# Performance work log

Measured on AMD Instinct MI355X. Metric: run time of the kernel, lower is better.

Reference implementation:

```python
import jax, jax.numpy as jnp
import numpy as np

H = 4            # heads
C = 64           # per-head dim (= hidden, PyG TransformerConv semantics)
HD = 64          # hidden_dim
L = 2            # num_layers
NT = 2           # node types: 0=task, 1=machine
ET = ((0, 1), (1, 0))  # edge types: (src_nt, dst_nt)
N = 16384        # nodes per type (== max_nodes -> simple pos-enc slice)
E = 262144       # edges per edge type


def _ln(x, g, b):
    mu = x.mean(-1, keepdims=True)
    var = ((x - mu) ** 2).mean(-1, keepdims=True)
    return (x - mu) * jax.lax.rsqrt(var + 1e-5) * g + b


def _tconv(x_src, x_dst, ei, Wq, bq, Wk, bk, Wv, bv, Ws, bs, Wb):
    # PyG TransformerConv: heads=H, out_channels=C, concat=False, beta=True
    n_dst = x_dst.shape[0]
    src, dst = ei[0], ei[1]
    q = (x_dst @ Wq + bq).reshape(-1, H, C)
    k = (x_src @ Wk + bk).reshape(-1, H, C)
    v = (x_src @ Wv + bv).reshape(-1, H, C)
    logits = jnp.einsum('ehc,ehc->eh', q[dst], k[src]) * (1.0 / float(np.sqrt(C)))  # [E,H]
    m = jax.ops.segment_max(logits, dst, num_segments=n_dst)          # [N,H] segment softmax
    ex = jnp.exp(logits - m[dst])
    denom = jax.ops.segment_sum(ex, dst, num_segments=n_dst)
    alpha = ex / denom[dst]                                            # [E,H]
    msg = (alpha[:, :, None] * v[src]).reshape(-1, H * C)              # [E,H*C]
    out = jax.ops.segment_sum(msg, dst, num_segments=n_dst)
    out = out.reshape(n_dst, H, C).mean(axis=1)                        # concat=False -> head mean
    r = x_dst @ Ws + bs                                                # lin_skip
    beta = jax.nn.sigmoid(jnp.concatenate([out, r, out - r], -1) @ Wb) # lin_beta, [N,1]
    return beta * r + (1.0 - beta) * out


def _forward(edge_index, x, W_in, b_in, type_emb, pos, Wq, bq, Wk, bk, Wv, bv,
             Wskip, bskip, Wbeta, ln_g, ln_b, ff_W1, ff_b1, ff_W2, ff_b2, W_out, b_out):
    # input proj + type embedding + positional encoding (num_nodes == max_nodes -> slice)
    h = [x[t] @ W_in[t] + b_in[t] + type_emb[t] + pos[t] for t in range(NT)]
    for l in range(L):
        hn = [jnp.zeros_like(h[0]), jnp.zeros_like(h[1])]
        for e, (s, d) in enumerate(ET):  # HeteroConv, aggr='sum'
            hn[d] = hn[d] + _tconv(h[s], h[d], edge_index[e],
                                   Wq[l, e], bq[l, e], Wk[l, e], bk[l, e],
                                   Wv[l, e], bv[l, e], Wskip[l, e], bskip[l, e], Wbeta[l, e])
        for t in range(NT):
            hr = _ln(h[t] + hn[t], ln_g[l, t], ln_b[l, t])
            ff = jax.nn.gelu(hr @ ff_W1[l, t] + ff_b1[l, t], approximate=False) @ ff_W2[l, t] + ff_b2[l, t]
            h[t] = hr + ff
    return jnp.stack([h[t] @ W_out[t] + b_out[t] for t in range(NT)])  # [NT,N,HD]


def setup_inputs() -> dict:
    key = jax.random.key(0)
    ks = jax.random.split(key, 16)
    w = lambda k, s: 0.02 * jax.random.normal(k, s, jnp.float32)
    NE = len(ET)
    return {
        'x': jax.random.normal(ks[0], (NT, N, HD), jnp.float32),
        'edge_index': jax.random.randint(ks[1], (NE, 2, E), 0, N, jnp.int32),
        'W_in': w(ks[2], (NT, HD, HD)), 'b_in': jnp.zeros((NT, HD), jnp.float32),
        'type_emb': w(ks[3], (NT, HD)),
        'pos': w(ks[4], (NT, N, HD)),
        'Wq': w(ks[5], (L, NE, HD, H * C)), 'bq': jnp.zeros((L, NE, H * C), jnp.float32),
        'Wk': w(ks[6], (L, NE, HD, H * C)), 'bk': jnp.zeros((L, NE, H * C), jnp.float32),
        'Wv': w(ks[7], (L, NE, HD, H * C)), 'bv': jnp.zeros((L, NE, H * C), jnp.float32),
        'Wskip': w(ks[8], (L, NE, HD, HD)), 'bskip': jnp.zeros((L, NE, HD), jnp.float32),
        'Wbeta': w(ks[9], (L, NE, 3 * HD, 1)),
        'ln_g': jnp.ones((L, NT, HD), jnp.float32), 'ln_b': jnp.zeros((L, NT, HD), jnp.float32),
        'ff_W1': w(ks[10], (L, NT, HD, 4 * HD)), 'ff_b1': jnp.zeros((L, NT, 4 * HD), jnp.float32),
        'ff_W2': w(ks[11], (L, NT, 4 * HD, HD)), 'ff_b2': jnp.zeros((L, NT, HD), jnp.float32),
        'W_out': w(ks[12], (NT, HD, HD)), 'b_out': jnp.zeros((NT, HD), jnp.float32),
    }


def reference(x, edge_index, W_in, b_in, type_emb, pos, Wq, bq, Wk, bk, Wv, bv,
              Wskip, bskip, Wbeta, ln_g, ln_b, ff_W1, ff_b1, ff_W2, ff_b2, W_out, b_out):
    return _forward(edge_index, x, W_in, b_in, type_emb, pos, Wq, bq, Wk, bk, Wv, bv,
                    Wskip, bskip, Wbeta, ln_g, ln_b, ff_W1, ff_b1, ff_W2, ff_b2, W_out, b_out)
```

## Files before the change

### kernel.cpp

```cpp
#include <hip/hip_runtime.h>
#include <math.h>

#define NN 16384
#define EE 262144

typedef __bf16 v8bf __attribute__((ext_vector_type(8)));
typedef __bf16 v4bf __attribute__((ext_vector_type(4)));
typedef float  v4f  __attribute__((ext_vector_type(4)));
typedef float  v2f  __attribute__((ext_vector_type(2)));

#define OFF_CNT     0
#define OFF_FILL    (2*NN)
#define OFF_ROWPTR  (4*NN)
#define OFF_COLSRC  98816
#define OFF_H       623104
#define OFF_HN      (OFF_H  + 2*NN*64)
#define OFF_Q       (OFF_HN + 2*NN*64)
#define OFF_KV      (OFF_Q  + 2*NN*128)
#define OFF_R       (OFF_KV + 2*NN*128)
#define OFF_WT      (OFF_R  + 2*NN*64)
#define OFF_WBP     (OFF_WT + 180224)
#define OFF_LNG     (OFF_WBP + 768)
#define OFF_LNB     (OFF_LNG + 256)


#define WT_Q   0
#define WT_K   65536
#define WT_V   131072
#define WT_S   196608
#define WT_IN  212992
#define WT_W1  221184
#define WT_W2  286720
#define WT_WO  352256

__device__ __forceinline__ float blo(unsigned u) { return __uint_as_float(u << 16); }
__device__ __forceinline__ float bhi(unsigned u) { return __uint_as_float(u & 0xffff0000u); }
__device__ __forceinline__ unsigned short f2b(float f) {
  __bf16 h = (__bf16)f;
  return *(unsigned short*)&h;
}

struct PrepDesc { const float* src; unsigned short* dst; int ksh; int total; int kperm; };
struct PrepPack { PrepDesc d[28]; };

__global__ __launch_bounds__(256) void prep_kernel(PrepPack p) {
  PrepDesc g = p.d[blockIdx.y];
  int idx = blockIdx.x * 256 + threadIdx.x;
  if (idx >= g.total) return;
  int K = 1 << g.ksh;
  int n = idx >> g.ksh;
  int k = idx & (K - 1);
  int N = g.total >> g.ksh;
  int kk = g.kperm ? (16 * (k & 3) + (k >> 2)) : k;
  g.dst[idx] = f2b(g.src[(size_t)kk * N + n]);
}

struct PermDesc { const float* src; float* dst; int total; };
struct PermPack { PermDesc d[3]; };

__global__ __launch_bounds__(256) void perm_kernel(PermPack p) {
  PermDesc g = p.d[blockIdx.y];
  int idx = blockIdx.x * 256 + threadIdx.x;
  if (idx >= g.total) return;
  int c = idx & 63;
  g.dst[(idx & ~63) + ((c & 15) << 2) + (c >> 4)] = g.src[idx];
}

__global__ void count_kernel(const int* __restrict__ ei, int* __restrict__ cnt) {
  int idx = blockIdx.x * 256 + threadIdx.x;
  if (idx >= 2 * EE) return;
  int et = idx >> 18;
  int j  = idx & (EE - 1);
  int dst = ei[et * 2 * EE + EE + j];
  atomicAdd(&cnt[et * NN + dst], 1);
}

__global__ __launch_bounds__(1024) void scan_kernel(const int* __restrict__ cnt,
                                                    int* __restrict__ rowptr,
                                                    int* __restrict__ fill) {
  int et = blockIdx.x;
  const int* c = cnt + et * NN;
  __shared__ int sums[1024];
  int tid = threadIdx.x;
  int base = tid * 16;
  int loc[16];
  int s = 0;
#pragma unroll
  for (int i = 0; i < 16; ++i) { loc[i] = s; s += c[base + i]; }
  sums[tid] = s;
  __syncthreads();
  for (int off = 1; off < 1024; off <<= 1) {
    int v = 0;
    if (tid >= off) v = sums[tid - off];
    __syncthreads();
    if (tid >= off) sums[tid] += v;
    __syncthreads();
  }
  int ebase = (tid == 0) ? 0 : sums[tid - 1];
  int* rp = rowptr + et * (NN + 1);
  int* fl = fill + et * NN;
#pragma unroll
  for (int i = 0; i < 16; ++i) {
    rp[base + i] = ebase + loc[i];
    fl[base + i] = ebase + loc[i];
  }
  if (tid == 1023) rp[NN] = sums[1023];
}

__global__ void scatter_kernel(const int* __restrict__ ei, int* __restrict__ fill,
                               int* __restrict__ colsrc) {
  int idx = blockIdx.x * 256 + threadIdx.x;
  if (idx >= 2 * EE) return;
  int et = idx >> 18;
  int j  = idx & (EE - 1);
  int src = ei[et * 2 * EE + j];
  int dst = ei[et * 2 * EE + EE + j];
  int pos = atomicAdd(&fill[et * NN + dst], 1);
  colsrc[et * EE + pos] = (et * NN + src) << 9;
}

struct GemmDesc {
  const float *A, *bias, *bias2, *add;
  const unsigned short* Bt;
  char* C;
  int Ncols, Cld, ntiles, gelu, otype;
};
struct GemmPack { GemmDesc d[8]; int nd; };

#define LDA 72

__global__ __launch_bounds__(256) void gemm_mfma(GemmPack p) {
  GemmDesc g = p.d[blockIdx.y];
  const int row0 = blockIdx.x * 128;
  const int tid = threadIdx.x;
  const int w = tid >> 6, lane = tid & 63;
  const int l16 = lane & 15, quad = lane >> 4;

  __shared__ __bf16 As[128 * LDA];
  __shared__ __bf16 Bs[64 * LDA];

#pragma unroll
  for (int it = 0; it < 8; ++it) {
    int fi = it * 256 + tid;
    int grow = fi >> 4;
    int kq = (fi & 15) << 2;
    float4 a = *(const float4*)(g.A + (size_t)(row0 + grow) * 64 + kq);
    v4bf c = { (__bf16)a.x, (__bf16)a.y, (__bf16)a.z, (__bf16)a.w };
    *(v4bf*)&As[grow * LDA + kq] = c;
  }

  const int brow = tid >> 2;
  const int bko  = (tid & 3) << 4;

  for (int ct0 = 0; ct0 < g.ntiles; ++ct0) {
    const int col0 = ct0 * 64;
    __syncthreads();
    {
      const unsigned short* bp = g.Bt + (size_t)(col0 + brow) * 64 + bko;
      uint4 b0 = *(const uint4*)(bp);
      uint4 b1 = *(const uint4*)(bp + 8);
      *(uint4*)&Bs[brow * LDA + bko] = b0;
      *(uint4*)&Bs[brow * LDA + bko + 8] = b1;
    }
    __syncthreads();

    v4f acc[2][4];
#pragma unroll
    for (int rt = 0; rt < 2; ++rt)
#pragma unroll
      for (int ct = 0; ct < 4; ++ct)
#pragma unroll
        for (int r = 0; r < 4; ++r) acc[rt][ct][r] = 0.f;

#pragma unroll
    for (int ks = 0; ks < 2; ++ks) {
      v8bf a0 = *(v8bf*)&As[(w * 32 + l16) * LDA + ks * 32 + quad * 8];
      v8bf a1 = *(v8bf*)&As[(w * 32 + 16 + l16) * LDA + ks * 32 + quad * 8];
#pragma unroll
      for (int ct = 0; ct < 4; ++ct) {
        v8bf bb = *(v8bf*)&Bs[(ct * 16 + l16) * LDA + ks * 32 + quad * 8];
        acc[0][ct] = __builtin_amdgcn_mfma_f32_16x16x32_bf16(a0, bb, acc[0][ct], 0, 0, 0);
        acc[1][ct] = __builtin_amdgcn_mfma_f32_16x16x32_bf16(a1, bb, acc[1][ct], 0, 0, 0);
      }
    }

    float bias_c[4];
#pragma unroll
    for (int ct = 0; ct < 4; ++ct) {
      int col = col0 + ct * 16 + l16;
      float b = g.bias ? g.bias[col] : 0.f;
      if (g.bias2) b += g.bias2[col];
      bias_c[ct] = b;
    }
#pragma unroll
    for (int rt = 0; rt < 2; ++rt)
#pragma unroll
      for (int r = 0; r < 4; ++r) {
        size_t row = row0 + w * 32 + rt * 16 + quad * 4 + r;
        char* cp = g.C + row * (size_t)g.Cld;
        if (g.otype == 0) {
          float vv[4];
#pragma unroll
          for (int ct = 0; ct < 4; ++ct) {
            int col = col0 + ct * 16 + l16;
            float v = acc[rt][ct][r] + bias_c[ct];
            if (g.add) v += g.add[row * g.Ncols + col];
            if (g.gelu) v = 0.5f * v * (1.f + erff(v * 0.70710678118654752f));
            vv[ct] = v;
          }
          float4 w4 = { vv[0], vv[1], vv[2], vv[3] };
          *(float4*)(cp + col0 * 4 + l16 * 16) = w4;
        } else if (g.otype == 1) {
          ushort4 wq;
          wq.x = f2b(acc[rt][0][r] + bias_c[0]);
          wq.y = f2b(acc[rt][1][r] + bias_c[1]);
          wq.z = f2b(acc[rt][2][r] + bias_c[2]);
          wq.w = f2b(acc[rt][3][r] + bias_c[3]);
          *(ushort4*)(cp + col0 * 2 + l16 * 8) = wq;
        } else {
          unsigned wv = 0;
#pragma unroll
          for (int ct = 0; ct < 4; ++ct) {
            float v = acc[rt][ct][r] + bias_c[ct];
            unsigned pk = __builtin_amdgcn_cvt_pk_fp8_f32(v, v, 0, false);
            wv |= (pk & 0xffu) << (8 * ct);
          }
          *(unsigned*)(cp + col0 + l16 * 4) = wv;
        }
      }
  }
}

struct FFPack {
  const float *HN;
  const unsigned short *W1t, *W2t, *Wot;
  const float *b1, *b2, *bout;
  float* H;
  float* outbuf;
};

__global__ __launch_bounds__(256) void ff_fused(FFPack p) {
  const int t = blockIdx.y;
  const int row0 = blockIdx.x * 64;
  const int tid = threadIdx.x;
  const int w = tid >> 6, lane = tid & 63;
  const int l16 = lane & 15, quad = lane >> 4;

  const float* A  = p.HN + ((size_t)t * NN) * 64;
  const unsigned short* W1t = p.W1t + (size_t)t * 16384;
  const unsigned short* W2t = p.W2t + (size_t)t * 16384;
  const float* b1 = p.b1 + t * 256;
  const float* b2 = p.b2 + t * 64;

  __shared__ __bf16 As[64 * LDA];
  __shared__ __bf16 A2[64 * LDA];
  __shared__ __bf16 B1s[64 * LDA];
  __shared__ __bf16 B2s[64 * LDA];

#pragma unroll
  for (int it = 0; it < 4; ++it) {
    int fi = it * 256 + tid;
    int grow = fi >> 4;
    int kq = (fi & 15) << 2;
    float4 a = *(const float4*)(A + (size_t)(row0 + grow) * 64 + kq);
    v4bf c = { (__bf16)a.x, (__bf16)a.y, (__bf16)a.z, (__bf16)a.w };
    *(v4bf*)&As[grow * LDA + kq] = c;
  }

  const int brow = tid >> 2;
  const int bko  = (tid & 3) << 4;

  v4f acc2[4];
#pragma unroll
  for (int ct = 0; ct < 4; ++ct)
#pragma unroll
    for (int r = 0; r < 4; ++r) acc2[ct][r] = 0.f;

  for (int c1 = 0; c1 < 4; ++c1) {
    {
      const unsigned short* bp1 = W1t + (size_t)(c1 * 64 + brow) * 64 + bko;
      uint4 u0 = *(const uint4*)(bp1);
      uint4 u1 = *(const uint4*)(bp1 + 8);
      *(uint4*)&B1s[brow * LDA + bko] = u0;
      *(uint4*)&B1s[brow * LDA + bko + 8] = u1;
      const unsigned short* bp2 = W2t + (size_t)brow * 256 + c1 * 64 + bko;
      uint4 u2 = *(const uint4*)(bp2);
      uint4 u3 = *(const uint4*)(bp2 + 8);
      *(uint4*)&B2s[brow * LDA + bko] = u2;
      *(uint4*)&B2s[brow * LDA + bko + 8] = u3;
    }
    __syncthreads();

    v4f acc1[4];
#pragma unroll
    for (int ct = 0; ct < 4; ++ct)
#pragma unroll
      for (int r = 0; r < 4; ++r) acc1[ct][r] = 0.f;
#pragma unroll
    for (int ks = 0; ks < 2; ++ks) {
      v8bf a = *(v8bf*)&As[(w * 16 + l16) * LDA + ks * 32 + quad * 8];
#pragma unroll
      for (int ct = 0; ct < 4; ++ct) {
        v8bf bb = *(v8bf*)&B1s[(ct * 16 + l16) * LDA + ks * 32 + quad * 8];
        acc1[ct] = __builtin_amdgcn_mfma_f32_16x16x32_bf16(a, bb, acc1[ct], 0, 0, 0);
      }
    }
#pragma unroll
    for (int ct = 0; ct < 4; ++ct) {
      float bb = b1[c1 * 64 + ct * 16 + l16];
#pragma unroll
      for (int r = 0; r < 4; ++r) {
        float v = acc1[ct][r] + bb;
        v = 0.5f * v * (1.f + erff(v * 0.70710678118654752f));
        A2[(w * 16 + quad * 4 + r) * LDA + ct * 16 + l16] = (__bf16)v;
      }
    }
#pragma unroll
    for (int ks = 0; ks < 2; ++ks) {
      v8bf a = *(v8bf*)&A2[(w * 16 + l16) * LDA + ks * 32 + quad * 8];
#pragma unroll
      for (int ct = 0; ct < 4; ++ct) {
        v8bf bb = *(v8bf*)&B2s[(ct * 16 + l16) * LDA + ks * 32 + quad * 8];
        acc2[ct] = __builtin_amdgcn_mfma_f32_16x16x32_bf16(a, bb, acc2[ct], 0, 0, 0);
      }
    }
    __syncthreads();
  }

  float b2c[4];
#pragma unroll
  for (int ct = 0; ct < 4; ++ct) b2c[ct] = b2[ct * 16 + l16];

  if (!p.outbuf) {
#pragma unroll
    for (int r = 0; r < 4; ++r) {
      size_t row = (size_t)t * NN + row0 + w * 16 + quad * 4 + r;
      float4 hn4 = *(const float4*)(p.HN + row * 64 + l16 * 4);
      float4 o4;
      o4.x = acc2[0][r] + b2c[0] + hn4.x;
      o4.y = acc2[1][r] + b2c[1] + hn4.y;
      o4.z = acc2[2][r] + b2c[2] + hn4.z;
      o4.w = acc2[3][r] + b2c[3] + hn4.w;
      *(float4*)(p.H + row * 64 + l16 * 4) = o4;
    }
    return;
  }

#pragma unroll
  for (int r = 0; r < 4; ++r) {
    int lrow = w * 16 + quad * 4 + r;
    size_t row = (size_t)t * NN + row0 + lrow;
    float4 hn4 = *(const float4*)(p.HN + row * 64 + l16 * 4);
    float hn[4] = { hn4.x, hn4.y, hn4.z, hn4.w };
#pragma unroll
    for (int ct = 0; ct < 4; ++ct) {
      int col = ct * 16 + l16;
      A2[lrow * LDA + col] = (__bf16)(acc2[ct][r] + b2c[ct] + hn[ct]);
    }
  }
  {
    const unsigned short* Wot = p.Wot + (size_t)t * 4096;
    const unsigned short* bp = Wot + (size_t)brow * 64 + bko;
    uint4 u0 = *(const uint4*)(bp);
    uint4 u1 = *(const uint4*)(bp + 8);
    *(uint4*)&B1s[brow * LDA + bko] = u0;
    *(uint4*)&B1s[brow * LDA + bko + 8] = u1;
  }
  __syncthreads();

  v4f acc3[4];
#pragma unroll
  for (int ct = 0; ct < 4; ++ct)
#pragma unroll
    for (int r = 0; r < 4; ++r) acc3[ct][r] = 0.f;
#pragma unroll
  for (int ks = 0; ks < 2; ++ks) {
    v8bf a = *(v8bf*)&A2[(w * 16 + l16) * LDA + ks * 32 + quad * 8];
#pragma unroll
    for (int ct = 0; ct < 4; ++ct) {
      v8bf bb = *(v8bf*)&B1s[(ct * 16 + l16) * LDA + ks * 32 + quad * 8];
      acc3[ct] = __builtin_amdgcn_mfma_f32_16x16x32_bf16(a, bb, acc3[ct], 0, 0, 0);
    }
  }
  const float* bo = p.bout + t * 64;
#pragma unroll
  for (int ct = 0; ct < 4; ++ct) {
    int col = ct * 16 + l16;
    float bb = bo[col];
#pragma unroll
    for (int r = 0; r < 4; ++r) {
      size_t row = (size_t)t * NN + row0 + w * 16 + quad * 4 + r;
      p.outbuf[row * 64 + col] = acc3[ct][r] + bb;
    }
  }
}

struct AggPack {
  const unsigned short *Q;
  const char *KV;
  const float *R;
  const float *Wb;
  const float *Hin;
  const float *lng, *lnb;
  float* outHR;
  const int *rowptr;
  const int *colsrc;
};

__global__ __launch_bounds__(256) void agg_kernel(AggPack p) {
  const int et = blockIdx.y, d = 1 - et;
  int wid = __builtin_amdgcn_readfirstlane(threadIdx.x >> 6);
  int lane = threadIdx.x & 63;
  int node = blockIdx.x * 4 + wid;
  int c4 = lane & 15;
  int cb = ((lane >> 4) << 6) + (c4 << 2);

  const int* rp = p.rowptr + et * (NN + 1);
  const int* cs = p.colsrc + et * EE;
  int start = rp[node], end = rp[node + 1];
  int len = end - start;
  int gnode = d * NN + node;

  uint2 qw = *(const uint2*)(p.Q + ((size_t)gnode << 8) + cb);
  float q0 = blo(qw.x) * 0.125f, q1 = bhi(qw.x) * 0.125f;
  float q2 = blo(qw.y) * 0.125f, q3 = bhi(qw.y) * 0.125f;

  int b[5];
#pragma unroll
  for (int i = 0; i <= 4; ++i) b[i] = start + ((len * i) >> 2);
  float dsum[4] = {0.f, 0.f, 0.f, 0.f};
  float acc[4][4];
#pragma unroll
  for (int s4 = 0; s4 < 4; ++s4)
#pragma unroll
    for (int c = 0; c < 4; ++c) acc[s4][c] = 0.f;

  int maxn = (len + 3) >> 2;
  int last = end - 1;
  for (int it = 0; it < maxn; ++it) {
#pragma unroll
    for (int s4 = 0; s4 < 4; ++s4) {
      int j = b[s4] + it;
      bool act = j < b[s4 + 1];
      int jc = act ? j : last;
      int off = cs[jc];
      const char* rowp = p.KV + off;
      unsigned kw = *(const unsigned*)(rowp + cb);
      unsigned vw = *(const unsigned*)(rowp + 256 + cb);
      v2f kl = __builtin_amdgcn_cvt_pk_f32_fp8((int)kw, false);
      v2f kh = __builtin_amdgcn_cvt_pk_f32_fp8((int)kw, true);
      float pd = q0 * kl[0] + q1 * kl[1] + q2 * kh[0] + q3 * kh[1];
      pd += __shfl_xor(pd, 1);
      pd += __shfl_xor(pd, 2);
      pd += __shfl_xor(pd, 4);
      pd += __shfl_xor(pd, 8);
      float wgt = act ? __expf(pd) : 0.f;
      v2f vl = __builtin_amdgcn_cvt_pk_f32_fp8((int)vw, false);
      v2f vh = __builtin_amdgcn_cvt_pk_f32_fp8((int)vw, true);
      dsum[s4] += wgt;
      acc[s4][0] += wgt * vl[0];
      acc[s4][1] += wgt * vl[1];
      acc[s4][2] += wgt * vh[0];
      acc[s4][3] += wgt * vh[1];
    }
  }
  float dn = (dsum[0] + dsum[1]) + (dsum[2] + dsum[3]);
  float o_[4];
#pragma unroll
  for (int i = 0; i < 4; ++i)
    o_[i] = (acc[0][i] + acc[1][i]) + (acc[2][i] + acc[3][i]);

  float inv = (len > 0) ? (0.25f / dn) : 0.f;
#pragma unroll
  for (int i = 0; i < 4; ++i) {
    float a = o_[i] * inv;
    a += __shfl_xor(a, 16);
    a += __shfl_xor(a, 32);
    o_[i] = a;
  }

  float4 r4 = *(const float4*)(p.R + (size_t)gnode * 64 + c4 * 4);
  float4 h4 = *(const float4*)(p.Hin + (size_t)gnode * 64 + c4 * 4);
  float rr[4] = { r4.x, r4.y, r4.z, r4.w };
  float hh[4] = { h4.x, h4.y, h4.z, h4.w };

  const float* wb = p.Wb + et * 192;
  float4 wo4 = *(const float4*)(wb + c4 * 4);
  float4 wr4 = *(const float4*)(wb + 64 + c4 * 4);
  float4 wd4 = *(const float4*)(wb + 128 + c4 * 4);
  float wo[4] = { wo4.x, wo4.y, wo4.z, wo4.w };
  float wr[4] = { wr4.x, wr4.y, wr4.z, wr4.w };
  float wd[4] = { wd4.x, wd4.y, wd4.z, wd4.w };
  float part = 0.f;
#pragma unroll
  for (int i = 0; i < 4; ++i)
    part += o_[i] * wo[i] + rr[i] * wr[i] + (o_[i] - rr[i]) * wd[i];
  part += __shfl_xor(part, 1);
  part += __shfl_xor(part, 2);
  part += __shfl_xor(part, 4);
  part += __shfl_xor(part, 8);
  float beta = 1.f / (1.f + __expf(-part));

  float y[4];
  float sa = 0.f, sb = 0.f;
#pragma unroll
  for (int i = 0; i < 4; ++i) {
    float v = hh[i] + beta * rr[i] + (1.f - beta) * o_[i];
    y[i] = v;
    sa += v;
    sb += v * v;
  }
  sa += __shfl_xor(sa, 1); sb += __shfl_xor(sb, 1);
  sa += __shfl_xor(sa, 2); sb += __shfl_xor(sb, 2);
  sa += __shfl_xor(sa, 4); sb += __shfl_xor(sb, 4);
  sa += __shfl_xor(sa, 8); sb += __shfl_xor(sb, 8);
  float mu = sa * (1.f / 64.f);
  float var = sb * (1.f / 64.f) - mu * mu;
  float rs = rsqrtf(var + 1e-5f);
  if (lane < 16) {
    float4 g4 = *(const float4*)(p.lng + d * 64 + c4 * 4);
    float4 bb4 = *(const float4*)(p.lnb + d * 64 + c4 * 4);
    float4 res;
    res.x = (y[0] - mu) * rs * g4.x + bb4.x;
    res.y = (y[1] - mu) * rs * g4.y + bb4.y;
    res.z = (y[2] - mu) * rs * g4.z + bb4.z;
    res.w = (y[3] - mu) * rs * g4.w + bb4.w;
    *(float4*)(p.outHR + (size_t)gnode * 64 + c4 * 4) = res;
  }
}

static void add_desc(GemmPack& p, const float* A, const unsigned short* Bt,
                     const float* bias, const float* bias2, const float* add,
                     void* C, int Nc, int Cld, int gelu, int otype) {
  GemmDesc& g = p.d[p.nd++];
  g.A = A; g.Bt = Bt; g.bias = bias; g.bias2 = bias2; g.add = add; g.C = (char*)C;
  g.Ncols = Nc; g.Cld = Cld; g.ntiles = Nc / 64;
  g.gelu = gelu; g.otype = otype;
}

extern "C" void kernel_launch(void* const* d_in, const int* in_sizes, int n_in,
                              void* d_out, int out_size, void* d_ws, size_t ws_size,
                              hipStream_t stream) {
  const float* x        = (const float*)d_in[0];
  const int*   ei       = (const int*)d_in[1];
  const float* W_in     = (const float*)d_in[2];
  const float* b_in     = (const float*)d_in[3];
  const float* type_emb = (const float*)d_in[4];
  const float* pos      = (const float*)d_in[5];
  const float* Wq       = (const float*)d_in[6];
  const float* bq       = (const float*)d_in[7];
  const float* Wk       = (const float*)d_in[8];
  const float* bk       = (const float*)d_in[9];
  const float* Wv       = (const float*)d_in[10];
  const float* bv       = (const float*)d_in[11];
  const float* Wskip    = (const float*)d_in[12];
  const float* bskip    = (const float*)d_in[13];
  const float* Wbeta    = (const float*)d_in[14];
  const float* ln_g     = (const float*)d_in[15];
  const float* ln_b     = (const float*)d_in[16];
  const float* ff_W1    = (const float*)d_in[17];
  const float* ff_b1    = (const float*)d_in[18];
  const float* ff_W2    = (const float*)d_in[19];
  const float* ff_b2    = (const float*)d_in[20];
  const float* W_out    = (const float*)d_in[21];
  const float* b_out    = (const float*)d_in[22];
  float* out = (float*)d_out;

  int*   wsi = (int*)d_ws;
  float* wsf = (float*)d_ws;
  int* cnt    = wsi + OFF_CNT;
  int* fill   = wsi + OFF_FILL;
  int* rowptr = wsi + OFF_ROWPTR;
  int* colsrc = wsi + OFF_COLSRC;
  float* H  = wsf + OFF_H;
  float* HN = wsf + OFF_HN;
  unsigned short* Qb = (unsigned short*)(wsf + OFF_Q);
  char* KVb = (char*)(wsf + OFF_KV);
  float* Rb = wsf + OFF_R;
  unsigned short* wt = (unsigned short*)(wsf + OFF_WT);
  float* wbp  = wsf + OFF_WBP;
  float* lngp = wsf + OFF_LNG;
  float* lnbp = wsf + OFF_LNB;

  {
    PrepPack pp{};
    int nd = 0;
    for (int we = 0; we < 4; ++we) {
      pp.d[nd++] = { Wq + (size_t)we * 16384, wt + WT_Q + we * 16384, 6, 16384, 1 };
      pp.d[nd++] = { Wk + (size_t)we * 16384, wt + WT_K + we * 16384, 6, 16384, 1 };
      pp.d[nd++] = { Wv + (size_t)we * 16384, wt + WT_V + we * 16384, 6, 16384, 1 };
      pp.d[nd++] = { Wskip + (size_t)we * 4096, wt + WT_S + we * 4096, 6, 4096, 1 };
      pp.d[nd++] = { ff_W1 + (size_t)we * 16384, wt + WT_W1 + we * 16384, 6, 16384, 1 };
      pp.d[nd++] = { ff_W2 + (size_t)we * 16384, wt + WT_W2 + we * 16384, 8, 16384, 0 };
    }
    for (int t = 0; t < 2; ++t) {
      pp.d[nd++] = { W_in + (size_t)t * 4096, wt + WT_IN + t * 4096, 6, 4096, 0 };
      pp.d[nd++] = { W_out + (size_t)t * 4096, wt + WT_WO + t * 4096, 6, 4096, 0 };
    }
    prep_kernel<<<dim3(64, nd), dim3(256), 0, stream>>>(pp);
  }
  {
    PermPack pm{};
    pm.d[0] = { Wbeta, wbp, 768 };
    pm.d[1] = { ln_g, lngp, 256 };
    pm.d[2] = { ln_b, lnbp, 256 };
    perm_kernel<<<dim3(3, 3), dim3(256), 0, stream>>>(pm);
  }

  hipMemsetAsync(cnt, 0, 2 * NN * sizeof(int), stream);
  count_kernel<<<dim3(2 * EE / 256), dim3(256), 0, stream>>>(ei, cnt);
  scan_kernel<<<dim3(2), dim3(1024), 0, stream>>>(cnt, rowptr, fill);
  scatter_kernel<<<dim3(2 * EE / 256), dim3(256), 0, stream>>>(ei, fill, colsrc);

  {
    GemmPack p{};
    for (int t = 0; t < 2; ++t)
      add_desc(p, x + (size_t)t * NN * 64, wt + WT_IN + t * 4096,
               b_in + t * 64, type_emb + t * 64, pos + (size_t)t * NN * 64,
               H + (size_t)t * NN * 64, 64, 256, 0, 0);
    gemm_mfma<<<dim3(128, p.nd), dim3(256), 0, stream>>>(p);
  }

  for (int l = 0; l < 2; ++l) {
    {
      GemmPack p{};
      for (int et = 0; et < 2; ++et) {
        int s = et, d = 1 - et;
        int we = l * 2 + et;
        const float* hs = H + (size_t)s * NN * 64;
        const float* hd = H + (size_t)d * NN * 64;
        add_desc(p, hd, wt + WT_Q + we * 16384, bq + we * 256,
                 nullptr, nullptr, (char*)Qb + (size_t)d * NN * 512, 256, 512, 0, 1);
        add_desc(p, hs, wt + WT_K + we * 16384, bk + we * 256,
                 nullptr, nullptr, KVb + (size_t)s * NN * 512, 256, 512, 0, 2);
        add_desc(p, hs, wt + WT_V + we * 16384, bv + we * 256,
                 nullptr, nullptr, KVb + (size_t)s * NN * 512 + 256, 256, 512, 0, 2);
        add_desc(p, hd, wt + WT_S + we * 4096, bskip + we * 64,
                 nullptr, nullptr, Rb + (size_t)d * NN * 64, 64, 256, 0, 0);
      }
      gemm_mfma<<<dim3(128, p.nd), dim3(256), 0, stream>>>(p);
    }

    AggPack ap;
    ap.Q = Qb; ap.KV = KVb; ap.R = Rb;
    ap.Wb = wbp + l * 2 * 192;
    ap.Hin = H;
    ap.lng = lngp + l * 128;
    ap.lnb = lnbp + l * 128;
    ap.outHR = HN;
    ap.rowptr = rowptr;
    ap.colsrc = colsrc;
    agg_kernel<<<dim3(NN / 4, 2), dim3(256), 0, stream>>>(ap);

    FFPack fp;
    fp.HN = HN;
    fp.W1t = wt + WT_W1 + l * 2 * 16384;
    fp.W2t = wt + WT_W2 + l * 2 * 16384;
    fp.Wot = wt + WT_WO;
    fp.b1 = ff_b1 + l * 2 * 256;
    fp.b2 = ff_b2 + l * 2 * 64;
    fp.bout = b_out;
    fp.H  = H;
    fp.outbuf = (l == 1) ? out : nullptr;
    ff_fused<<<dim3(NN / 64, 2), dim3(256), 0, stream>>>(fp);
  }
}
```

Baseline: 321.7 us.

## Merge prep launches, vectorize CSR build, and use direct-to-LDS swizzled B loads

Folds the permutation kernel and the counter memset into the single prep kernel, which cuts two launches. The count and scatter kernels now read four edges per thread with int4 loads. The GEMM B tile is loaded with global_load_lds into an unpadded LDS buffer. Weights are pre-swizzled with an XOR pattern so the LDS reads avoid bank conflicts. The swizzled layout only holds for the weights written in modes 4 and 5, so every GEMM that reads Bt must be given a matching layout.

```diff
diff --git a/kernel.cpp b/kernel.cpp
--- a/kernel.cpp
+++ b/kernel.cpp
@@ -40,39 +40,43 @@
   return *(unsigned short*)&h;
 }
 
-struct PrepDesc { const float* src; unsigned short* dst; int ksh; int total; int kperm; };
-struct PrepPack { PrepDesc d[28]; };
+struct PrepDesc { const float* src; void* dst; int ksh; int total; int mode; };
+struct PrepPack { PrepDesc d[34]; };
 
 __global__ __launch_bounds__(256) void prep_kernel(PrepPack p) {
   PrepDesc g = p.d[blockIdx.y];
   int idx = blockIdx.x * 256 + threadIdx.x;
   if (idx >= g.total) return;
+  if (g.mode == 3) { ((int*)g.dst)[idx] = 0; return; }
+  if (g.mode == 2) {
+    int c = idx & 63;
+    ((float*)g.dst)[(idx & ~63) + ((c & 15) << 2) + (c >> 4)] = g.src[idx];
+    return;
+  }
   int K = 1 << g.ksh;
   int n = idx >> g.ksh;
   int k = idx & (K - 1);
   int N = g.total >> g.ksh;
-  int kk = g.kperm ? (16 * (k & 3) + (k >> 2)) : k;
-  g.dst[idx] = f2b(g.src[(size_t)kk * N + n]);
-}
-
-struct PermDesc { const float* src; float* dst; int total; };
-struct PermPack { PermDesc d[3]; };
-
-__global__ __launch_bounds__(256) void perm_kernel(PermPack p) {
-  PermDesc g = p.d[blockIdx.y];
-  int idx = blockIdx.x * 256 + threadIdx.x;
-  if (idx >= g.total) return;
-  int c = idx & 63;
-  g.dst[(idx & ~63) + ((c & 15) << 2) + (c >> 4)] = g.src[idx];
+  if (g.mode >= 4) {
+    int c = k >> 3, oo = k & 7;
+    int ks = ((c ^ (n & 7)) << 3) | oo;
+    int kk = (g.mode == 5) ? (16 * (ks & 3) + (ks >> 2)) : ks;
+    ((unsigned short*)g.dst)[idx] = f2b(g.src[(size_t)kk * N + n]);
+    return;
+  }
+  int kk = (g.mode == 1) ? (16 * (k & 3) + (k >> 2)) : k;
+  ((unsigned short*)g.dst)[idx] = f2b(g.src[(size_t)kk * N + n]);
 }
 
 __global__ void count_kernel(const int* __restrict__ ei, int* __restrict__ cnt) {
   int idx = blockIdx.x * 256 + threadIdx.x;
-  if (idx >= 2 * EE) return;
-  int et = idx >> 18;
-  int j  = idx & (EE - 1);
-  int dst = ei[et * 2 * EE + EE + j];
-  atomicAdd(&cnt[et * NN + dst], 1);
+  int et = idx >> 16;
+  int j4 = (idx & 65535) << 2;
+  int4 dv = *(const int4*)(ei + (size_t)et * 2 * EE + EE + j4);
+  atomicAdd(&cnt[et * NN + dv.x], 1);
+  atomicAdd(&cnt[et * NN + dv.y], 1);
+  atomicAdd(&cnt[et * NN + dv.z], 1);
+  atomicAdd(&cnt[et * NN + dv.w], 1);
 }
 
 __global__ __launch_bounds__(1024) void scan_kernel(const int* __restrict__ cnt,
@@ -110,13 +114,18 @@
 __global__ void scatter_kernel(const int* __restrict__ ei, int* __restrict__ fill,
                                int* __restrict__ colsrc) {
   int idx = blockIdx.x * 256 + threadIdx.x;
-  if (idx >= 2 * EE) return;
-  int et = idx >> 18;
-  int j  = idx & (EE - 1);
-  int src = ei[et * 2 * EE + j];
-  int dst = ei[et * 2 * EE + EE + j];
-  int pos = atomicAdd(&fill[et * NN + dst], 1);
-  colsrc[et * EE + pos] = (et * NN + src) << 9;
+  int et = idx >> 16;
+  int j4 = (idx & 65535) << 2;
+  const int* eb = ei + (size_t)et * 2 * EE;
+  int4 sv = *(const int4*)(eb + j4);
+  int4 dv = *(const int4*)(eb + EE + j4);
+  int* fl = fill + et * NN;
+  int* csb = colsrc + et * EE;
+  int pos;
+  pos = atomicAdd(&fl[dv.x], 1); csb[pos] = (et * NN + sv.x) << 9;
+  pos = atomicAdd(&fl[dv.y], 1); csb[pos] = (et * NN + sv.y) << 9;
+  pos = atomicAdd(&fl[dv.z], 1); csb[pos] = (et * NN + sv.z) << 9;
+  pos = atomicAdd(&fl[dv.w], 1); csb[pos] = (et * NN + sv.w) << 9;
 }
 
 struct GemmDesc {
@@ -137,7 +146,7 @@
   const int l16 = lane & 15, quad = lane >> 4;
 
   __shared__ __bf16 As[128 * LDA];
-  __shared__ __bf16 Bs[64 * LDA];
+  __shared__ __bf16 Bs[64 * 64];
 
 #pragma unroll
   for (int it = 0; it < 8; ++it) {
@@ -149,18 +158,18 @@
     *(v4bf*)&As[grow * LDA + kq] = c;
   }
 
-  const int brow = tid >> 2;
-  const int bko  = (tid & 3) << 4;
-
   for (int ct0 = 0; ct0 < g.ntiles; ++ct0) {
     const int col0 = ct0 * 64;
     __syncthreads();
     {
-      const unsigned short* bp = g.Bt + (size_t)(col0 + brow) * 64 + bko;
-      uint4 b0 = *(const uint4*)(bp);
-      uint4 b1 = *(const uint4*)(bp + 8);
-      *(uint4*)&Bs[brow * LDA + bko] = b0;
-      *(uint4*)&Bs[brow * LDA + bko + 8] = b1;
+      const char* gb = (const char*)g.Bt + (size_t)ct0 * 8192;
+      char* lb = (char*)Bs;
+      __builtin_amdgcn_global_load_lds(
+          (const unsigned int*)(gb + w * 2048 + lane * 16),
+          (unsigned int*)(lb + w * 2048), 16, 0, 0);
+      __builtin_amdgcn_global_load_lds(
+          (const unsigned int*)(gb + w * 2048 + 1024 + lane * 16),
+          (unsigned int*)(lb + w * 2048 + 1024), 16, 0, 0);
     }
     __syncthreads();
 
@@ -178,7 +187,9 @@
       v8bf a1 = *(v8bf*)&As[(w * 32 + 16 + l16) * LDA + ks * 32 + quad * 8];
 #pragma unroll
       for (int ct = 0; ct < 4; ++ct) {
-        v8bf bb = *(v8bf*)&Bs[(ct * 16 + l16) * LDA + ks * 32 + quad * 8];
+        int rr = ct * 16 + l16;
+        int sw = (((ks * 4 + quad) ^ (rr & 7)) << 4);
+        v8bf bb = *(const v8bf*)((const char*)Bs + rr * 128 + sw);
         acc[0][ct] = __builtin_amdgcn_mfma_f32_16x16x32_bf16(a0, bb, acc[0][ct], 0, 0, 0);
         acc[1][ct] = __builtin_amdgcn_mfma_f32_16x16x32_bf16(a1, bb, acc[1][ct], 0, 0, 0);
       }
@@ -586,31 +597,28 @@
     PrepPack pp{};
     int nd = 0;
     for (int we = 0; we < 4; ++we) {
-      pp.d[nd++] = { Wq + (size_t)we * 16384, wt + WT_Q + we * 16384, 6, 16384, 1 };
-      pp.d[nd++] = { Wk + (size_t)we * 16384, wt + WT_K + we * 16384, 6, 16384, 1 };
-      pp.d[nd++] = { Wv + (size_t)we * 16384, wt + WT_V + we * 16384, 6, 16384, 1 };
-      pp.d[nd++] = { Wskip + (size_t)we * 4096, wt + WT_S + we * 4096, 6, 4096, 1 };
+      pp.d[nd++] = { Wq + (size_t)we * 16384, wt + WT_Q + we * 16384, 6, 16384, 5 };
+      pp.d[nd++] = { Wk + (size_t)we * 16384, wt + WT_K + we * 16384, 6, 16384, 5 };
+      pp.d[nd++] = { Wv + (size_t)we * 16384, wt + WT_V + we * 16384, 6, 16384, 5 };
+      pp.d[nd++] = { Wskip + (size_t)we * 4096, wt + WT_S + we * 4096, 6, 4096, 5 };
       pp.d[nd++] = { ff_W1 + (size_t)we * 16384, wt + WT_W1 + we * 16384, 6, 16384, 1 };
       pp.d[nd++] = { ff_W2 + (size_t)we * 16384, wt + WT_W2 + we * 16384, 8, 16384, 0 };
     }
     for (int t = 0; t < 2; ++t) {
-      pp.d[nd++] = { W_in + (size_t)t * 4096, wt + WT_IN + t * 4096, 6, 4096, 0 };
+      pp.d[nd++] = { W_in + (size_t)t * 4096, wt + WT_IN + t * 4096, 6, 4096, 4 };
       pp.d[nd++] = { W_out + (size_t)t * 4096, wt + WT_WO + t * 4096, 6, 4096, 0 };
     }
+    pp.d[nd++] = { Wbeta, wbp, 0, 768, 2 };
+    pp.d[nd++] = { ln_g, lngp, 0, 256, 2 };
+    pp.d[nd++] = { ln_b, lnbp, 0, 256, 2 };
+    pp.d[nd++] = { nullptr, cnt, 0, 16384, 3 };
+    pp.d[nd++] = { nullptr, cnt + 16384, 0, 16384, 3 };
     prep_kernel<<<dim3(64, nd), dim3(256), 0, stream>>>(pp);
   }
-  {
-    PermPack pm{};
-    pm.d[0] = { Wbeta, wbp, 768 };
-    pm.d[1] = { ln_g, lngp, 256 };
-    pm.d[2] = { ln_b, lnbp, 256 };
-    perm_kernel<<<dim3(3, 3), dim3(256), 0, stream>>>(pm);
-  }
-
-  hipMemsetAsync(cnt, 0, 2 * NN * sizeof(int), stream);
-  count_kernel<<<dim3(2 * EE / 256), dim3(256), 0, stream>>>(ei, cnt);
+
+  count_kernel<<<dim3(2 * EE / 1024), dim3(256), 0, stream>>>(ei, cnt);
   scan_kernel<<<dim3(2), dim3(1024), 0, stream>>>(cnt, rowptr, fill);
-  scatter_kernel<<<dim3(2 * EE / 256), dim3(256), 0, stream>>>(ei, fill, colsrc);
+  scatter_kernel<<<dim3(2 * EE / 1024), dim3(256), 0, stream>>>(ei, fill, colsrc);
 
   {
     GemmPack p{};
```

Result: no change. 325.1 us (+1.0%).
